# Kernel optimization log

Hardware: AMD Instinct MI355X
Metric: run time of the kernel (lower is better)

Reference implementation:

```python
import jax, jax.numpy as jnp
import numpy as np

B, S, D = 2, 2048, 1024
H = 16
HD = D // H  # 64
EPS = 1e-5
ROPE_BASE = 10000.0


def _rope_cos_sin(seq_len, head_dim, dtype):
    # inv_freq over even channel indices, standard rotate-half RoPE
    inv_freq = 1.0 / (ROPE_BASE ** (jnp.arange(0, head_dim, 2, dtype=jnp.float32) / head_dim))
    ang = jnp.arange(seq_len, dtype=jnp.float32)[:, None] * inv_freq[None, :]  # [S, HD/2]
    emb = jnp.concatenate([ang, ang], axis=-1)  # [S, HD]
    return jnp.cos(emb).astype(dtype), jnp.sin(emb).astype(dtype)


def _rotate_half(x):
    x1, x2 = jnp.split(x, 2, axis=-1)
    return jnp.concatenate([-x2, x1], axis=-1)


def setup_inputs() -> dict:
    key = jax.random.key(0)
    ks = jax.random.split(key, 5)
    std = 0.023  # default init_method: normal(mean=0, std=0.023)
    return {
        "hidden_states": jax.random.normal(ks[0], (B, S, D), dtype=jnp.float32),
        "ln_gamma": jnp.ones((D,), dtype=jnp.float32),
        "ln_beta": jnp.zeros((D,), dtype=jnp.float32),
        "qkv_weight": jax.random.normal(ks[1], (3 * D, D), dtype=jnp.float32) * std,
        "qkv_bias": jax.random.normal(ks[2], (3 * D,), dtype=jnp.float32) * std,
        "proj_weight": jax.random.normal(ks[3], (D, D), dtype=jnp.float32) * std,
        "proj_bias": jax.random.normal(ks[4], (D,), dtype=jnp.float32) * std,
    }


def reference(hidden_states, ln_gamma, ln_beta, qkv_weight, qkv_bias, proj_weight, proj_bias):
    b, s, d = hidden_states.shape
    # --- input LayerNorm ---
    mu = jnp.mean(hidden_states, axis=-1, keepdims=True)
    var = jnp.mean(jnp.square(hidden_states - mu), axis=-1, keepdims=True)
    x = (hidden_states - mu) * jax.lax.rsqrt(var + EPS) * ln_gamma + ln_beta

    # --- fused QKV projection (interleaved per-head q,k,v) ---
    qkv = x @ qkv_weight.T + qkv_bias  # [B,S,3D]
    qkv = qkv.reshape(b, s, H, 3, HD)
    q, k, v = qkv[..., 0, :], qkv[..., 1, :], qkv[..., 2, :]  # each [B,S,H,HD]

    # --- RoPE on q and k ---
    cos, sin = _rope_cos_sin(s, HD, q.dtype)  # [S,HD]
    cos = cos[None, :, None, :]
    sin = sin[None, :, None, :]
    q = q * cos + _rotate_half(q) * sin
    k = k * cos + _rotate_half(k) * sin

    # --- causal scaled-dot-product attention ---
    scale = 1.0 / jnp.sqrt(jnp.asarray(HD, dtype=q.dtype))
    scores = jnp.einsum("bqhd,bkhd->bhqk", q, k) * scale  # [B,H,S,S]
    causal = jnp.tril(jnp.ones((s, s), dtype=bool))
    scores = jnp.where(causal[None, None, :, :], scores, jnp.finfo(scores.dtype).min)
    probs = jax.nn.softmax(scores, axis=-1)
    ctx = jnp.einsum("bhqk,bkhd->bqhd", probs, v).reshape(b, s, d)

    # --- output projection ---
    return ctx @ proj_weight.T + proj_bias
```

## Files before the change

### kernel.cpp

```cpp
#include <hip/hip_runtime.h>
#include <math.h>

#define B_  2
#define S_  2048
#define D_  1024
#define H_  16
#define HD_ 64
#define BS_ (B_ * S_)

typedef __bf16 bf16_t;
typedef __bf16 bf16x8 __attribute__((ext_vector_type(8)));
typedef __bf16 bf16x4 __attribute__((ext_vector_type(4)));
typedef float  f32x4  __attribute__((ext_vector_type(4)));
typedef short  s16x4  __attribute__((ext_vector_type(4)));

#define QSCALE 0.18033688011112042f
#define FREQC  0.28782313662425575f

__device__ __forceinline__ void async_ld16(const bf16_t* g, bf16_t* l)
{
    __builtin_amdgcn_global_load_lds(
        (const __attribute__((address_space(1))) void*)g,
        (__attribute__((address_space(3))) void*)l,
        16, 0, 0);
}

__device__ __forceinline__ int chunk_base(int t)
{
    if (t < 8)  return t;
    if (t < 16) return 8 + 2 * (t - 8);
    if (t < 24) return 24 + 3 * (t - 16);
    return 48 + 4 * (t - 24);
}

__global__ __launch_bounds__(256) void ln_cvt(const float* __restrict__ x,
                                              const float* __restrict__ gamma,
                                              const float* __restrict__ beta,
                                              bf16_t* __restrict__ y,
                                              const float* __restrict__ wa,
                                              const float* __restrict__ wb,
                                              bf16_t* __restrict__ oa,
                                              bf16_t* __restrict__ ob)
{
    if (blockIdx.x >= BS_) {
        int idx = (blockIdx.x - BS_) * 256 + threadIdx.x;
        const int NA = 3 * D_ * D_ / 4;
        if (idx < NA) {
            float4 v = ((const float4*)wa)[idx];
            bf16x4 p;
            p[0] = (bf16_t)v.x; p[1] = (bf16_t)v.y; p[2] = (bf16_t)v.z; p[3] = (bf16_t)v.w;
            ((bf16x4*)oa)[idx] = p;
        } else {
            int j = idx - NA;
            float4 v = ((const float4*)wb)[j];
            bf16x4 p;
            p[0] = (bf16_t)v.x; p[1] = (bf16_t)v.y; p[2] = (bf16_t)v.z; p[3] = (bf16_t)v.w;
            ((bf16x4*)ob)[j] = p;
        }
        return;
    }
    int row = blockIdx.x;
    float4 v = ((const float4*)(x + (size_t)row * D_))[threadIdx.x];
    float sum = v.x + v.y + v.z + v.w;
    float sq  = v.x * v.x + v.y * v.y + v.z * v.z + v.w * v.w;
#pragma unroll
    for (int off = 32; off > 0; off >>= 1) {
        sum += __shfl_down(sum, off);
        sq  += __shfl_down(sq, off);
    }
    __shared__ float s_sum[4], s_sq[4];
    int wave = threadIdx.x >> 6;
    if ((threadIdx.x & 63) == 0) { s_sum[wave] = sum; s_sq[wave] = sq; }
    __syncthreads();
    float tsum = s_sum[0] + s_sum[1] + s_sum[2] + s_sum[3];
    float tsq  = s_sq[0] + s_sq[1] + s_sq[2] + s_sq[3];
    float mean = tsum * (1.0f / D_);
    float var  = tsq * (1.0f / D_) - mean * mean;
    float rstd = rsqrtf(var + 1e-5f);
    float4 g = ((const float4*)gamma)[threadIdx.x];
    float4 b = ((const float4*)beta)[threadIdx.x];
    bf16x4 o;
    o[0] = (bf16_t)((v.x - mean) * rstd * g.x + b.x);
    o[1] = (bf16_t)((v.y - mean) * rstd * g.y + b.y);
    o[2] = (bf16_t)((v.z - mean) * rstd * g.z + b.z);
    o[3] = (bf16_t)((v.w - mean) * rstd * g.w + b.w);
    *(bf16x4*)&y[(size_t)row * D_ + threadIdx.x * 4] = o;
}

template<int MODE, int TM>
__global__ __launch_bounds__(256) void gemm_bf16(const bf16_t* __restrict__ A,
                                                 const bf16_t* __restrict__ W,
                                                 const float* __restrict__ bias,
                                                 float* __restrict__ outf,
                                                 bf16_t* __restrict__ qout,
                                                 bf16_t* __restrict__ kout,
                                                 bf16_t* __restrict__ vout,
                                                 int M, int N, int K)
{
    constexpr int ASZ = TM * 32;
    constexpr int BUF = ASZ + 4096;
    constexpr int SMEM = (MODE == 1) ? 18432 : 2 * BUF;
    constexpr int MI = (TM == 128) ? 4 : 2;
    __shared__ bf16_t smem[SMEM];
    const int bm = blockIdx.y * TM, bn = blockIdx.x * 128;
    const int tid = threadIdx.x;
    const int wave = tid >> 6, lane = tid & 63;
    const int ln16 = lane & 15, quad = lane >> 4;
    const int wr = (wave >> 1) * (TM / 2), wc = (wave & 1) * 64;
    const int slot_a = (quad ^ (ln16 & 3)) * 8;

    f32x4 acc[MI][4];
#pragma unroll
    for (int i = 0; i < MI; i++)
#pragma unroll
        for (int j = 0; j < 4; j++) acc[i][j] = (f32x4){0.f, 0.f, 0.f, 0.f};

#pragma unroll
    for (int j = 0; j < TM / 64; j++) {
        int e = j * 256 + tid;
        int r = e >> 2, cg = ((e & 3) ^ (r & 3)) * 8;
        async_ld16(&A[(size_t)(bm + r) * K + cg], smem + e * 8);
    }
#pragma unroll
    for (int j = 0; j < 2; j++) {
        int e = j * 256 + tid;
        int r = e >> 2, cg = ((e & 3) ^ (r & 3)) * 8;
        async_ld16(&W[(size_t)(bn + r) * K + cg], smem + ASZ + e * 8);
    }
    __syncthreads();

    for (int k0 = 0, it = 0; k0 < K; k0 += 32, it++) {
        const bf16_t* cur = smem + (it & 1) * BUF;
        bf16_t* nxt = smem + ((it & 1) ^ 1) * BUF;
        if (k0 + 32 < K) {
#pragma unroll
            for (int j = 0; j < TM / 64; j++) {
                int e = j * 256 + tid;
                int r = e >> 2, cg = ((e & 3) ^ (r & 3)) * 8;
                async_ld16(&A[(size_t)(bm + r) * K + k0 + 32 + cg], nxt + e * 8);
            }
#pragma unroll
            for (int j = 0; j < 2; j++) {
                int e = j * 256 + tid;
                int r = e >> 2, cg = ((e & 3) ^ (r & 3)) * 8;
                async_ld16(&W[(size_t)(bn + r) * K + k0 + 32 + cg], nxt + ASZ + e * 8);
            }
        }

        bf16x8 af[MI], bf[4];
#pragma unroll
        for (int mi = 0; mi < MI; mi++)
            af[mi] = *(const bf16x8*)&cur[(wr + mi * 16 + ln16) * 32 + slot_a];
#pragma unroll
        for (int ni = 0; ni < 4; ni++)
            bf[ni] = *(const bf16x8*)&cur[ASZ + (wc + ni * 16 + ln16) * 32 + slot_a];
#pragma unroll
        for (int mi = 0; mi < MI; mi++)
#pragma unroll
            for (int ni = 0; ni < 4; ni++)
                acc[mi][ni] = __builtin_amdgcn_mfma_f32_16x16x32_bf16(
                    af[mi], bf[ni], acc[mi][ni], 0, 0, 0);

        __syncthreads();
    }

#pragma unroll
    for (int ni = 0; ni < 4; ni++) {
        float bb = bias[bn + wc + ni * 16 + ln16];
#pragma unroll
        for (int mi = 0; mi < MI; mi++)
#pragma unroll
            for (int r = 0; r < 4; r++) acc[mi][ni][r] += bb;
    }

    if (MODE == 0) {
#pragma unroll
        for (int ni = 0; ni < 4; ni++) {
            int n = bn + wc + ni * 16 + ln16;
#pragma unroll
            for (int mi = 0; mi < MI; mi++)
#pragma unroll
                for (int r = 0; r < 4; r++)
                    outf[(size_t)(bm + wr + mi * 16 + quad * 4 + r) * N + n] = acc[mi][ni][r];
        }
    } else {
        const int n64 = (bn + wc) >> 6;
        const int t = n64 % 3, h = n64 / 3;
        bf16_t* T = smem + wave * (64 * 72);
        if (t == 2) {
#pragma unroll
            for (int mi = 0; mi < 4; mi++) {
#pragma unroll
                for (int ni = 0; ni < 4; ni++) {
                    bf16x4 pk;
#pragma unroll
                    for (int r = 0; r < 4; r++) pk[r] = (bf16_t)acc[mi][ni][r];
                    *(bf16x4*)&T[(ni * 16 + ln16) * 72 + mi * 16 + quad * 4] = pk;
                }
            }
            int m0 = bm + wr;
            int bi = m0 >> 11, s0g = m0 & (S_ - 1);
#pragma unroll
            for (int e = lane; e < 512; e += 64) {
                int hd_l = e >> 3, c8 = (e & 7) << 3;
                *(bf16x8*)&vout[((size_t)(bi * H_ + h) * HD_ + hd_l) * S_ + s0g + c8] =
                    *(const bf16x8*)&T[hd_l * 72 + c8];
            }
        } else {
            float fr0 = __expf(-(float)ln16 * FREQC);
            float fr1 = __expf(-(float)(16 + ln16) * FREQC);
            float sc = (t == 0) ? QSCALE : 1.0f;
#pragma unroll
            for (int mi = 0; mi < 4; mi++) {
#pragma unroll
                for (int r = 0; r < 4; r++) {
                    int m = bm + wr + mi * 16 + quad * 4 + r;
                    float s = (float)(m & (S_ - 1));
                    float sn0, cs0, sn1, cs1;
                    __sincosf(s * fr0, &sn0, &cs0);
                    __sincosf(s * fr1, &sn1, &cs1);
                    int rowo = (mi * 16 + quad * 4 + r) * 72;
                    float x1 = acc[mi][0][r], x2 = acc[mi][2][r];
                    T[rowo + ln16]      = (bf16_t)((x1 * cs0 - x2 * sn0) * sc);
                    T[rowo + 32 + ln16] = (bf16_t)((x2 * cs0 + x1 * sn0) * sc);
                    x1 = acc[mi][1][r]; x2 = acc[mi][3][r];
                    T[rowo + 16 + ln16] = (bf16_t)((x1 * cs1 - x2 * sn1) * sc);
                    T[rowo + 48 + ln16] = (bf16_t)((x2 * cs1 + x1 * sn1) * sc);
                }
            }
            bf16_t* dst = (t == 0) ? qout : kout;
#pragma unroll
            for (int e = lane; e < 512; e += 64) {
                int row_l = e >> 3, c8 = (e & 7) << 3;
                int m = bm + wr + row_l;
                int b = m >> 11, s = m & (S_ - 1);
                *(bf16x8*)&dst[((size_t)(b * H_ + h) * S_ + s) * HD_ + c8] =
                    *(const bf16x8*)&T[row_l * 72 + c8];
            }
        }
    }
}

__global__ __launch_bounds__(256) void attn_p1(const bf16_t* __restrict__ q_buf,
                                               const bf16_t* __restrict__ k_buf,
                                               const bf16_t* __restrict__ v_t,
                                               bf16_t* __restrict__ part_o,
                                               float* __restrict__ part_l)
{
    __shared__ bf16_t KS[2][4096];
    __shared__ bf16_t VS[2][4096];

    const int h = blockIdx.y, b = blockIdx.z;
    const int xx = 79 - blockIdx.x;
    int t, c;
    if (xx < 8)       { t = xx;                c = 0; }
    else if (xx < 24) { int y = xx - 8;  t = 8 + (y >> 1);  c = y & 1; }
    else if (xx < 48) { int y = xx - 24; int q = y / 3; t = 16 + q; c = y - 3 * q; }
    else              { int y = xx - 48; t = 24 + (y >> 2); c = y & 3; }
    const int k0c = c * 8;
    const int k1c = min(t, k0c + 7);

    const int tid = threadIdx.x;
    const int wave = tid >> 6, lane = tid & 63;
    const int ln16 = lane & 15, quad = lane >> 4;
    const int w0 = t * 64 + wave * 16;
    const int s7 = ln16 & 7;

    const bf16_t* qb = q_buf + (size_t)(b * H_ + h) * S_ * HD_;
    const bf16_t* kb = k_buf + (size_t)(b * H_ + h) * S_ * HD_;
    const bf16_t* vb = v_t  + (size_t)(b * H_ + h) * HD_ * S_;

    const int e0 = tid, e1 = tid + 256;
    const int r0 = e0 >> 3, c0 = ((e0 & 7) ^ (r0 & 7)) * 8;
    const int r1 = e1 >> 3, c1 = ((e1 & 7) ^ (r1 & 7)) * 8;

    bf16x8 qf[2];
#pragma unroll
    for (int kc = 0; kc < 2; kc++)
        qf[kc] = *(const bf16x8*)&qb[(size_t)(w0 + ln16) * HD_ + kc * 32 + quad * 8];

    f32x4 o[4];
#pragma unroll
    for (int mi = 0; mi < 4; mi++) o[mi] = (f32x4){0.f, 0.f, 0.f, 0.f};
    float l_i = 0.f;

    async_ld16(&kb[(size_t)(k0c * 64 + r0) * HD_ + c0], &KS[0][e0 * 8]);
    async_ld16(&kb[(size_t)(k0c * 64 + r1) * HD_ + c1], &KS[0][e1 * 8]);
    async_ld16(&vb[(size_t)r0 * S_ + k0c * 64 + c0], &VS[0][e0 * 8]);
    async_ld16(&vb[(size_t)r1 * S_ + k0c * 64 + c1], &VS[0][e1 * 8]);
    __syncthreads();

    for (int kt = k0c; kt <= k1c; kt++) {
        const int cb = (kt - k0c) & 1;
        if (kt < k1c) {
            const int nb = cb ^ 1, kn = kt + 1;
            async_ld16(&kb[(size_t)(kn * 64 + r0) * HD_ + c0], &KS[nb][e0 * 8]);
            async_ld16(&kb[(size_t)(kn * 64 + r1) * HD_ + c1], &KS[nb][e1 * 8]);
            async_ld16(&vb[(size_t)r0 * S_ + kn * 64 + c0], &VS[nb][e0 * 8]);
            async_ld16(&vb[(size_t)r1 * S_ + kn * 64 + c1], &VS[nb][e1 * 8]);
        }

        const bf16_t* Kc = &KS[cb][0];
        const bf16_t* Vc = &VS[cb][0];

        f32x4 st[4];
#pragma unroll
        for (int cbx = 0; cbx < 4; cbx++) st[cbx] = (f32x4){0.f, 0.f, 0.f, 0.f};
#pragma unroll
        for (int kc = 0; kc < 2; kc++)
#pragma unroll
            for (int cbx = 0; cbx < 4; cbx++) {
                bf16x8 kf = *(const bf16x8*)&Kc[(cbx * 16 + ln16) * 64 + ((kc * 4 + quad) ^ s7) * 8];
                st[cbx] = __builtin_amdgcn_mfma_f32_16x16x32_bf16(kf, qf[kc], st[cbx], 0, 0, 0);
            }

        if (kt == t) {
            int q_g = w0 + ln16;
#pragma unroll
            for (int cbx = 0; cbx < 4; cbx++) {
                int key0 = kt * 64 + cbx * 16 + quad * 4;
#pragma unroll
                for (int r = 0; r < 4; r++)
                    if (key0 + r > q_g) st[cbx][r] = -1e30f;
            }
        }

#pragma unroll
        for (int cbx = 0; cbx < 4; cbx++)
#pragma unroll
            for (int r = 0; r < 4; r++) {
                float p = exp2f(st[cbx][r]);
                st[cbx][r] = p;
                l_i += p;
            }

        s16x4 pf4[4];
#pragma unroll
        for (int cbx = 0; cbx < 4; cbx++) {
            union { bf16x4 hv; s16x4 sv; } u;
#pragma unroll
            for (int r = 0; r < 4; r++) u.hv[r] = (bf16_t)st[cbx][r];
            pf4[cbx] = u.sv;
        }

#pragma unroll
        for (int cbx = 0; cbx < 4; cbx++) {
            int slot = ((cbx * 2 + (quad >> 1)) ^ s7) * 8 + (quad & 1) * 4;
#pragma unroll
            for (int mi = 0; mi < 4; mi++) {
                union { bf16x4 hv; s16x4 sv; } uv;
                uv.hv = *(const bf16x4*)&Vc[(mi * 16 + ln16) * 64 + slot];
                o[mi] = __builtin_amdgcn_mfma_f32_16x16x16bf16_1k(uv.sv, pf4[cbx], o[mi], 0, 0, 0);
            }
        }

        __syncthreads();
    }

    l_i += __shfl_xor(l_i, 16);
    l_i += __shfl_xor(l_i, 32);

    const size_t pidx = (size_t)(b * H_ + h) * 80 + chunk_base(t) + c;
    bf16_t* po = part_o + pidx * 4096;
    const int q_l = wave * 16 + ln16;
#pragma unroll
    for (int mi = 0; mi < 4; mi++) {
        bf16x4 pk;
#pragma unroll
        for (int r = 0; r < 4; r++) pk[r] = (bf16_t)o[mi][r];
        *(bf16x4*)&po[q_l * 64 + mi * 16 + quad * 4] = pk;
    }
    if (quad == 0)
        part_l[pidx * 64 + q_l] = l_i;
}

__global__ __launch_bounds__(256) void attn_p2(const bf16_t* __restrict__ part_o,
                                               const float* __restrict__ part_l,
                                               bf16_t* __restrict__ ctx)
{
    const int t = blockIdx.x, h = blockIdx.y, b = blockIdx.z;
    const int nch = (t >> 3) + 1;
    const size_t p0 = (size_t)(b * H_ + h) * 80 + chunk_base(t);
    const int q_l = threadIdx.x >> 2;
    const int hg = (threadIdx.x & 3) * 16;

    float L = 0.f;
    float f0[8] = {0,0,0,0,0,0,0,0}, f1[8] = {0,0,0,0,0,0,0,0};
#pragma unroll
    for (int i = 0; i < 4; i++) {
        if (i < nch) {
            L += part_l[(p0 + i) * 64 + q_l];
            const bf16_t* oi = part_o + (p0 + i) * 4096 + q_l * 64 + hg;
            bf16x8 v0 = *(const bf16x8*)oi;
            bf16x8 v1 = *(const bf16x8*)(oi + 8);
#pragma unroll
            for (int j = 0; j < 8; j++) {
                f0[j] += (float)v0[j];
                f1[j] += (float)v1[j];
            }
        }
    }
    float invL = 1.0f / L;
    bf16x8 out0, out1;
#pragma unroll
    for (int j = 0; j < 8; j++) {
        out0[j] = (bf16_t)(f0[j] * invL);
        out1[j] = (bf16_t)(f1[j] * invL);
    }
    bf16_t* dst = &ctx[(size_t)(b * S_ + t * 64 + q_l) * D_ + h * HD_ + hg];
    *(bf16x8*)dst = out0;
    *(bf16x8*)(dst + 8) = out1;
}

extern "C" void kernel_launch(void* const* d_in, const int* in_sizes, int n_in,
                              void* d_out, int out_size, void* d_ws, size_t ws_size,
                              hipStream_t stream)
{
    const float* hidden = (const float*)d_in[0];
    const float* gamma  = (const float*)d_in[1];
    const float* beta   = (const float*)d_in[2];
    const float* qkv_w  = (const float*)d_in[3];
    const float* qkv_b  = (const float*)d_in[4];
    const float* proj_w = (const float*)d_in[5];
    const float* proj_b = (const float*)d_in[6];
    float* out = (float*)d_out;

    char* ws = (char*)d_ws;
    const size_t MB = 1024 * 1024;
    bf16_t* x_ln = (bf16_t*)(ws);
    bf16_t* wq   = (bf16_t*)(ws +  8 * MB);
    bf16_t* wp   = (bf16_t*)(ws + 14 * MB);
    bf16_t* qbf  = (bf16_t*)(ws + 16 * MB);
    bf16_t* kbf  = (bf16_t*)(ws + 24 * MB);
    bf16_t* vtb  = (bf16_t*)(ws + 32 * MB);
    bf16_t* ctx  = (bf16_t*)(ws + 40 * MB);
    bf16_t* po   = (bf16_t*)(ws + 48 * MB);
    float*  pl   = (float*)(ws + 68 * MB);

    ln_cvt<<<BS_ + 4096, 256, 0, stream>>>(hidden, gamma, beta, x_ln,
                                           qkv_w, proj_w, wq, wp);
    gemm_bf16<1, 128><<<dim3(24, 32), 256, 0, stream>>>(
        x_ln, wq, qkv_b, nullptr, qbf, kbf, vtb, BS_, 3 * D_, D_);
    attn_p1<<<dim3(80, H_, B_), 256, 0, stream>>>(qbf, kbf, vtb, po, pl);
    attn_p2<<<dim3(32, H_, B_), 256, 0, stream>>>(po, pl, ctx);
    gemm_bf16<0, 64><<<dim3(8, 64), 256, 0, stream>>>(
        ctx, wp, proj_b, out, nullptr, nullptr, nullptr, BS_, D_, D_);
}
```

Baseline: 194.0 us.

## Process two query tiles per attention block to share K/V loads

Each attn_p1 block now runs 8 waves (512 threads) covering 128 query rows instead of 64, so one K/V tile staged in LDS serves two query tiles. Each thread now issues one async load per buffer instead of two. The causal mask is applied to every key tile at or past the wave's own diagonal, and the grid is halved. This cuts global-to-LDS traffic and load instructions per query. In exchange, the lower query tile of each pair computes one fully masked key tile, and the larger blocks may reduce occupancy.

```diff
diff --git a/kernel.cpp b/kernel.cpp
--- a/kernel.cpp
+++ b/kernel.cpp
@@ -241,7 +241,7 @@
     }
 }
 
-__global__ __launch_bounds__(256) void attn_p1(const bf16_t* __restrict__ q_buf,
+__global__ __launch_bounds__(512) void attn_p1(const bf16_t* __restrict__ q_buf,
                                                const bf16_t* __restrict__ k_buf,
                                                const bf16_t* __restrict__ v_t,
                                                bf16_t* __restrict__ part_o,
@@ -251,28 +251,27 @@
     __shared__ bf16_t VS[2][4096];
 
     const int h = blockIdx.y, b = blockIdx.z;
-    const int xx = 79 - blockIdx.x;
-    int t, c;
-    if (xx < 8)       { t = xx;                c = 0; }
-    else if (xx < 24) { int y = xx - 8;  t = 8 + (y >> 1);  c = y & 1; }
-    else if (xx < 48) { int y = xx - 24; int q = y / 3; t = 16 + q; c = y - 3 * q; }
-    else              { int y = xx - 48; t = 24 + (y >> 2); c = y & 3; }
+    const int xx = 39 - blockIdx.x;
+    int T, c;
+    if (xx < 4)       { T = xx;                 c = 0; }
+    else if (xx < 12) { int y = xx - 4;  T = 4 + (y >> 1); c = y & 1; }
+    else if (xx < 24) { int y = xx - 12; int q = y / 3; T = 8 + q; c = y - 3 * q; }
+    else              { int y = xx - 24; T = 12 + (y >> 2); c = y & 3; }
     const int k0c = c * 8;
-    const int k1c = min(t, k0c + 7);
+    const int k1c = min(2 * T + 1, k0c + 7);
 
     const int tid = threadIdx.x;
     const int wave = tid >> 6, lane = tid & 63;
     const int ln16 = lane & 15, quad = lane >> 4;
-    const int w0 = t * 64 + wave * 16;
+    const int w0 = T * 128 + wave * 16;
+    const int dt = w0 >> 6;
     const int s7 = ln16 & 7;
 
     const bf16_t* qb = q_buf + (size_t)(b * H_ + h) * S_ * HD_;
     const bf16_t* kb = k_buf + (size_t)(b * H_ + h) * S_ * HD_;
     const bf16_t* vb = v_t  + (size_t)(b * H_ + h) * HD_ * S_;
 
-    const int e0 = tid, e1 = tid + 256;
-    const int r0 = e0 >> 3, c0 = ((e0 & 7) ^ (r0 & 7)) * 8;
-    const int r1 = e1 >> 3, c1 = ((e1 & 7) ^ (r1 & 7)) * 8;
+    const int r0 = tid >> 3, c0 = ((tid & 7) ^ (r0 & 7)) * 8;
 
     bf16x8 qf[2];
 #pragma unroll
@@ -284,20 +283,16 @@
     for (int mi = 0; mi < 4; mi++) o[mi] = (f32x4){0.f, 0.f, 0.f, 0.f};
     float l_i = 0.f;
 
-    async_ld16(&kb[(size_t)(k0c * 64 + r0) * HD_ + c0], &KS[0][e0 * 8]);
-    async_ld16(&kb[(size_t)(k0c * 64 + r1) * HD_ + c1], &KS[0][e1 * 8]);
-    async_ld16(&vb[(size_t)r0 * S_ + k0c * 64 + c0], &VS[0][e0 * 8]);
-    async_ld16(&vb[(size_t)r1 * S_ + k0c * 64 + c1], &VS[0][e1 * 8]);
+    async_ld16(&kb[(size_t)(k0c * 64 + r0) * HD_ + c0], &KS[0][tid * 8]);
+    async_ld16(&vb[(size_t)r0 * S_ + k0c * 64 + c0], &VS[0][tid * 8]);
     __syncthreads();
 
     for (int kt = k0c; kt <= k1c; kt++) {
         const int cb = (kt - k0c) & 1;
         if (kt < k1c) {
             const int nb = cb ^ 1, kn = kt + 1;
-            async_ld16(&kb[(size_t)(kn * 64 + r0) * HD_ + c0], &KS[nb][e0 * 8]);
-            async_ld16(&kb[(size_t)(kn * 64 + r1) * HD_ + c1], &KS[nb][e1 * 8]);
-            async_ld16(&vb[(size_t)r0 * S_ + kn * 64 + c0], &VS[nb][e0 * 8]);
-            async_ld16(&vb[(size_t)r1 * S_ + kn * 64 + c1], &VS[nb][e1 * 8]);
+            async_ld16(&kb[(size_t)(kn * 64 + r0) * HD_ + c0], &KS[nb][tid * 8]);
+            async_ld16(&vb[(size_t)r0 * S_ + kn * 64 + c0], &VS[nb][tid * 8]);
         }
 
         const bf16_t* Kc = &KS[cb][0];
@@ -314,7 +309,7 @@
                 st[cbx] = __builtin_amdgcn_mfma_f32_16x16x32_bf16(kf, qf[kc], st[cbx], 0, 0, 0);
             }
 
-        if (kt == t) {
+        if (kt >= dt) {
             int q_g = w0 + ln16;
 #pragma unroll
             for (int cbx = 0; cbx < 4; cbx++) {
@@ -360,9 +355,10 @@
     l_i += __shfl_xor(l_i, 16);
     l_i += __shfl_xor(l_i, 32);
 
-    const size_t pidx = (size_t)(b * H_ + h) * 80 + chunk_base(t) + c;
+    const int t_tile = dt;
+    const size_t pidx = (size_t)(b * H_ + h) * 80 + chunk_base(t_tile) + c;
     bf16_t* po = part_o + pidx * 4096;
-    const int q_l = wave * 16 + ln16;
+    const int q_l = (wave & 3) * 16 + ln16;
 #pragma unroll
     for (int mi = 0; mi < 4; mi++) {
         bf16x4 pk;
@@ -441,7 +437,7 @@
                                            qkv_w, proj_w, wq, wp);
     gemm_bf16<1, 128><<<dim3(24, 32), 256, 0, stream>>>(
         x_ln, wq, qkv_b, nullptr, qbf, kbf, vtb, BS_, 3 * D_, D_);
-    attn_p1<<<dim3(80, H_, B_), 256, 0, stream>>>(qbf, kbf, vtb, po, pl);
+    attn_p1<<<dim3(40, H_, B_), 512, 0, stream>>>(qbf, kbf, vtb, po, pl);
     attn_p2<<<dim3(32, H_, B_), 256, 0, stream>>>(po, pl, ctx);
     gemm_bf16<0, 64><<<dim3(8, 64), 256, 0, stream>>>(
         ctx, wp, proj_b, out, nullptr, nullptr, nullptr, BS_, D_, D_);
```

Measured after the change: 186.6 us. 1.04x faster.
